# Performance work log

Measured on AMD Instinct MI355X. Metric: run time of the kernel, lower is better.

## Reference

```python
import jax, jax.numpy as jnp
import numpy as np

TEMPERATURE = 1.0
EPS = 1e-7
MAX_NORM = 0.9  # project points strictly inside the Poincare ball


def _project_ball(x):
    n = jnp.linalg.norm(x, axis=-1, keepdims=True)
    return x * jnp.minimum(1.0, MAX_NORM / jnp.maximum(n, EPS))


def setup_inputs() -> dict:
    key = jax.random.key(0)
    kq, kk, kv = jax.random.split(key, 3)
    B, Nq, Nk, D, V = 8, 2048, 2048, 64, 128
    queries = _project_ball(jax.random.normal(kq, (B, Nq, D), dtype=jnp.float32))
    keys = _project_ball(jax.random.normal(kk, (B, Nk, D), dtype=jnp.float32))
    values = jax.random.normal(kv, (B, Nk, V), dtype=jnp.float32)
    return {"queries": queries, "keys": keys, "values": values}


def _poincare_pairwise_dist(x, y):
    # x: (B,N,D), y: (B,M,D) -> (B,N,M) geodesic distances on the Poincare ball
    x2 = jnp.sum(x * x, axis=-1)            # (B,N)
    y2 = jnp.sum(y * y, axis=-1)            # (B,M)
    xy = jnp.einsum('bnd,bmd->bnm', x, y)   # (B,N,M)
    sq = jnp.maximum(x2[:, :, None] + y2[:, None, :] - 2.0 * xy, 0.0)
    denom = jnp.maximum((1.0 - x2)[:, :, None] * (1.0 - y2)[:, None, :], EPS)
    arg = 1.0 + 2.0 * sq / denom
    return jnp.arccosh(jnp.maximum(arg, 1.0 + EPS))


def reference(queries, keys, values):
    distances = _poincare_pairwise_dist(queries, keys)          # (B,Nq,Nk)
    scores = -(distances * distances) / TEMPERATURE
    attention_weights = jax.nn.softmax(scores, axis=-1)         # (B,Nq,Nk)
    output = jnp.einsum('bnm,bmv->bnv', attention_weights, values)  # (B,Nq,V)
    return output, attention_weights
```

## Files before the change

### kernel.cpp

```cpp
#include <hip/hip_runtime.h>
#include <math.h>

#define BB 8
#define NQ 2048
#define NK 2048
#define DD 64
#define VV 128
#define EPSF 1e-7f
#define NT3 (NK / 64)
#define FIXROWS 1024

typedef _Float16 half_t;
typedef half_t half8 __attribute__((ext_vector_type(8)));
typedef float  floatx4 __attribute__((ext_vector_type(4)));

__device__ __forceinline__ float score_exp(float x2, float y2, float xy)
{
    float sq = fmaf(-2.f, xy, x2 + y2);
    float dn = fmaxf((1.f - x2) * (1.f - y2), EPSF);
    float tt = fmaxf(2.f * sq * __builtin_amdgcn_rcpf(dn), EPSF);
    float u  = tt + __builtin_amdgcn_sqrtf(fmaf(tt, tt, tt + tt));
    float L  = __log2f(1.f + u);
    return __builtin_amdgcn_exp2f(-0.6931471805599453f * L * L);
}

__device__ __forceinline__ half8 cvt8(float4 a, float4 b)
{
    half8 h;
    h[0] = (half_t)a.x; h[1] = (half_t)a.y; h[2] = (half_t)a.z; h[3] = (half_t)a.w;
    h[4] = (half_t)b.x; h[5] = (half_t)b.y; h[6] = (half_t)b.z; h[7] = (half_t)b.w;
    return h;
}

__device__ __forceinline__ size_t khg_idx(int b, int tile, int f, int l)
{ return (((size_t)b * NT3 + tile) * 8 + f) * 64 + l; }
__device__ __forceinline__ size_t vhg_idx(int b, int tile, int f, int l)
{ return (((size_t)b * NT3 + tile) * 16 + f) * 64 + l; }

__device__ __forceinline__ int ssh_byte(int row, int col)
{
    return ((row << 7) + (col << 1)) ^ ((row & 7) << 4);
}

__global__ __launch_bounds__(256)
void k0_prep(const float* __restrict__ Q, const float* __restrict__ Kp,
             const float* __restrict__ V, half8* __restrict__ Khg,
             half8* __restrict__ Vhg, float* __restrict__ y2g,
             float* __restrict__ x2g, float* __restrict__ wsY,
             float* __restrict__ wsX)
{
    __shared__ float sVt[64 * VV];

    const int t = threadIdx.x, b = blockIdx.y, tile = blockIdx.x;
    const int kt = tile * 64;
    const float* Kb = Kp + (size_t)b * NK * DD;
    const float* Qb = Q  + (size_t)b * NQ * DD;
    const float* Vb = V  + (size_t)b * NK * VV;

#pragma unroll
    for (int i = 0; i < 8; ++i)
        ((float4*)sVt)[t + i * 256] = ((const float4*)(Vb + (size_t)kt * VV))[t + i * 256];

#pragma unroll
    for (int i = 0; i < 2; ++i) {
        int s = t + i * 256, f = s >> 6, l = s & 63;
        int krow = kt + (f >> 1) * 16 + (l & 15);
        int dcol = (f & 1) * 32 + (l >> 4) * 8;
        const float4* kp = (const float4*)(Kb + (size_t)krow * DD + dcol);
        Khg[khg_idx(b, tile, f, l)] = cvt8(kp[0], kp[1]);
    }
    if (t < 64) {
        const float4* kr = (const float4*)(Kb + (size_t)(kt + t) * DD);
        float s = 0.f;
#pragma unroll
        for (int i = 0; i < 16; ++i) {
            float4 v = kr[i];
            s = fmaf(v.x,v.x,s); s = fmaf(v.y,v.y,s);
            s = fmaf(v.z,v.z,s); s = fmaf(v.w,v.w,s);
        }
        y2g[(size_t)b * NK + kt + t] = s;
        if (b == 0) wsY[kt + t] = s;
    } else if (t < 128) {
        int r = t - 64;
        const float4* qr = (const float4*)(Qb + (size_t)(kt + r) * DD);
        float s = 0.f;
#pragma unroll
        for (int i = 0; i < 16; ++i) {
            float4 v = qr[i];
            s = fmaf(v.x,v.x,s); s = fmaf(v.y,v.y,s);
            s = fmaf(v.z,v.z,s); s = fmaf(v.w,v.w,s);
        }
        x2g[(size_t)b * NQ + kt + r] = s;
        if (b == 0) wsX[kt + r] = s;
    }
    __syncthreads();

#pragma unroll
    for (int i = 0; i < 4; ++i) {
        int s = t + i * 256, f = s >> 6, l = s & 63;
        int krow_l = (f & 1) * 32 + (l >> 4) * 8;
        int vcol   = (f >> 1) * 16 + (l & 15);
        half8 h;
#pragma unroll
        for (int j = 0; j < 8; ++j) h[j] = (half_t)sVt[(krow_l + j) * VV + vcol];
        Vhg[vhg_idx(b, tile, f, l)] = h;
    }
}

__global__ __launch_bounds__(512, 4)
void k_main(const float* __restrict__ Q, const half8* __restrict__ Khg,
            const half8* __restrict__ Vhg, const float* __restrict__ y2g,
            const float* __restrict__ x2g, float* __restrict__ W,
            float* __restrict__ O, float* __restrict__ RS)
{
    __shared__ half_t sSh[32 * 64];
    __shared__ float  y2k[NK];
    __shared__ float  part[4][32];
    __shared__ float  rsumS[32];

    const int t = threadIdx.x, w = t >> 6, lane = t & 63;
    const int n = lane & 15, quad = lane >> 4;
    const int qh = w & 1, kq = w >> 1;

    const int bid = blockIdx.x;
    const int swz = (bid & 7) * 64 + (bid >> 3);
    const int b = swz >> 6, qb = (swz & 63) * 32;
    const bool wskip = (b == 0) && (qb < FIXROWS);

    const float* Qb = Q + (size_t)b * NQ * DD;

    ((float4*)y2k)[t] = ((const float4*)(y2g + (size_t)b * NK))[t];

    half8 af[2];
#pragma unroll
    for (int ds = 0; ds < 2; ++ds) {
        const float4* qp = (const float4*)(Qb + (size_t)(qb + qh*16 + n) * DD + ds*32 + quad*8);
        af[ds] = cvt8(qp[0], qp[1]);
    }
    float x2r[4];
#pragma unroll
    for (int r = 0; r < 4; ++r)
        x2r[r] = x2g[(size_t)b * NQ + qb + qh * 16 + quad * 4 + r];
    __syncthreads();

    float srow[4] = {0.f, 0.f, 0.f, 0.f};

    half8 bf[8];
#pragma unroll
    for (int f = 0; f < 8; ++f) bf[f] = Khg[khg_idx(b, kq * 8, f, lane)];

#pragma unroll 1
    for (int kt0 = 0; kt0 < 512; kt0 += 64) {
        const bool pf = (kt0 + 64) < 512;
        half8 bfn[8];
        if (pf) {
#pragma unroll
            for (int f = 0; f < 8; ++f)
                bfn[f] = Khg[khg_idx(b, kq * 8 + ((kt0 + 64) >> 6), f, lane)];
        }

        floatx4 acc4[4] = {};
#pragma unroll
        for (int nt = 0; nt < 4; ++nt)
#pragma unroll
            for (int ds = 0; ds < 2; ++ds)
                acc4[nt] = __builtin_amdgcn_mfma_f32_16x16x32_f16(
                    af[ds], bf[nt * 2 + ds], acc4[nt], 0, 0, 0);

#pragma unroll
        for (int nt = 0; nt < 4; ++nt) {
            int lcol = kq * 512 + kt0 + nt * 16 + n;
            float y2 = y2k[lcol];
#pragma unroll
            for (int r = 0; r < 4; ++r)
                srow[r] += score_exp(x2r[r], y2, acc4[nt][r]);
        }
        if (pf) {
#pragma unroll
            for (int f = 0; f < 8; ++f) bf[f] = bfn[f];
        }
    }

#pragma unroll
    for (int off = 1; off < 16; off <<= 1)
#pragma unroll
        for (int r = 0; r < 4; ++r) srow[r] += __shfl_xor(srow[r], off);
    if (n == 0)
#pragma unroll
        for (int r = 0; r < 4; ++r) part[kq][qh * 16 + quad * 4 + r] = srow[r];
    __syncthreads();
    if (t < 32) {
        float s = (part[0][t] + part[1][t]) + (part[2][t] + part[3][t]);
        RS[(size_t)b * NQ + qb + t] = s;
        rsumS[t] = s;
    }
    __syncthreads();

    float rlr[4];
#pragma unroll
    for (int r = 0; r < 4; ++r)
        rlr[r] = __builtin_amdgcn_rcpf(rsumS[qh * 16 + quad * 4 + r]);

    float* Wb = W + (size_t)b * NQ * NK;
    floatx4 acc[2] = {};

    half8 kf[2];
#pragma unroll
    for (int ds = 0; ds < 2; ++ds) kf[ds] = Khg[khg_idx(b, 0, kq * 2 + ds, lane)];

#pragma unroll 1
    for (int tt = 0; tt < NT3; ++tt) {
        const bool pf = (tt + 1) < NT3;

        floatx4 a2 = {};
        a2 = __builtin_amdgcn_mfma_f32_16x16x32_f16(af[0], kf[0], a2, 0, 0, 0);
        a2 = __builtin_amdgcn_mfma_f32_16x16x32_f16(af[1], kf[1], a2, 0, 0, 0);

        half8 vf[4];
        vf[0] = Vhg[vhg_idx(b, tt, kq * 2,           lane)];
        vf[1] = Vhg[vhg_idx(b, tt, kq * 2 + 1,       lane)];
        vf[2] = Vhg[vhg_idx(b, tt, (kq + 4) * 2,     lane)];
        vf[3] = Vhg[vhg_idx(b, tt, (kq + 4) * 2 + 1, lane)];
        half8 kfn[2];
        if (pf) {
#pragma unroll
            for (int ds = 0; ds < 2; ++ds)
                kfn[ds] = Khg[khg_idx(b, tt + 1, kq * 2 + ds, lane)];
        }

        {
            int col  = kq * 16 + n;
            int gcol = tt * 64 + col;
            float y2 = y2k[gcol];
#pragma unroll
            for (int r = 0; r < 4; ++r) {
                float e  = score_exp(x2r[r], y2, a2[r]);
                float wv = e * rlr[r];
                int row = qh * 16 + quad * 4 + r;
                if (!wskip)
                    __builtin_nontemporal_store(wv, Wb + (size_t)(qb + row) * NK + gcol);
                *(half_t*)((char*)sSh + ssh_byte(row, col)) = (half_t)wv;
            }
        }
        __syncthreads();

        const int row2 = qh * 16 + n;
        half8 a0 = *(const half8*)((const char*)sSh + ssh_byte(row2, quad * 8));
        half8 a1 = *(const half8*)((const char*)sSh + ssh_byte(row2, 32 + quad * 8));
        acc[0] = __builtin_amdgcn_mfma_f32_16x16x32_f16(a0, vf[0], acc[0], 0, 0, 0);
        acc[0] = __builtin_amdgcn_mfma_f32_16x16x32_f16(a1, vf[1], acc[0], 0, 0, 0);
        acc[1] = __builtin_amdgcn_mfma_f32_16x16x32_f16(a0, vf[2], acc[1], 0, 0, 0);
        acc[1] = __builtin_amdgcn_mfma_f32_16x16x32_f16(a1, vf[3], acc[1], 0, 0, 0);
        __syncthreads();

        if (pf) { kf[0] = kfn[0]; kf[1] = kfn[1]; }
    }

    float* Ob = O + (size_t)b * NQ * VV;
#pragma unroll
    for (int ci = 0; ci < 2; ++ci) {
        int c = kq + ci * 4;
#pragma unroll
        for (int r = 0; r < 4; ++r)
            Ob[(size_t)(qb + qh * 16 + quad * 4 + r) * VV + c * 16 + n]
                = acc[ci][r];
    }
}

__global__ __launch_bounds__(256)
void k4_wfix(const float* __restrict__ Q, const float* __restrict__ Kp,
             const float* __restrict__ RS, const float* __restrict__ wsY,
             const float* __restrict__ wsX, float* __restrict__ W)
{
    __shared__ half8 sB[8 * 64];
    __shared__ float y2k[128];
    __shared__ float x2q[32];

    const int t = threadIdx.x, w = t >> 6, lane = t & 63;
    const int n = lane & 15, quad = lane >> 4;
    const int qh = w & 1, kn = w >> 1;
    const int qb = blockIdx.x * 32;
    const int kz = blockIdx.y * 128;

    if (t < 128) y2k[t] = wsY[kz + t];
    if (t < 32)  x2q[t] = wsX[qb + t];
    __syncthreads();

    half8 af[2];
#pragma unroll
    for (int ds = 0; ds < 2; ++ds) {
        const float4* qp = (const float4*)(Q + (size_t)(qb + qh*16 + n) * DD + ds*32 + quad*8);
        af[ds] = cvt8(qp[0], qp[1]);
    }
    float x2r[4], rlr[4];
#pragma unroll
    for (int r = 0; r < 4; ++r) {
        int row = qb + qh * 16 + quad * 4 + r;
        x2r[r] = x2q[qh * 16 + quad * 4 + r];
        rlr[r] = __builtin_amdgcn_rcpf(RS[row]);
    }

#pragma unroll 1
    for (int kt = 0; kt < 128; kt += 64) {
        __syncthreads();
#pragma unroll
        for (int i = 0; i < 2; ++i) {
            int s = t + i * 256, f = s >> 6, l = s & 63;
            int krow = kz + kt + (f >> 1) * 16 + (l & 15);
            int dcol = (f & 1) * 32 + (l >> 4) * 8;
            const float4* kp = (const float4*)(Kp + (size_t)krow * DD + dcol);
            sB[f * 64 + l] = cvt8(kp[0], kp[1]);
        }
        __syncthreads();

        floatx4 a2[2] = {};
#pragma unroll
        for (int nt = 0; nt < 2; ++nt)
#pragma unroll
            for (int ds = 0; ds < 2; ++ds)
                a2[nt] = __builtin_amdgcn_mfma_f32_16x16x32_f16(
                    af[ds], sB[((kn * 2 + nt) * 2 + ds) * 64 + lane], a2[nt], 0, 0, 0);

#pragma unroll
        for (int nt = 0; nt < 2; ++nt) {
            int col = kn * 32 + nt * 16 + n;
            float y2 = y2k[kt + col];
#pragma unroll
            for (int r = 0; r < 4; ++r) {
                float e = score_exp(x2r[r], y2, a2[nt][r]);
                int row = qh * 16 + quad * 4 + r;
                W[(size_t)(qb + row) * NK + kz + kt + col] = e * rlr[r];
            }
        }
    }
}

extern "C" void kernel_launch(void* const* d_in, const int* in_sizes, int n_in,
                              void* d_out, int out_size, void* d_ws, size_t ws_size,
                              hipStream_t stream)
{
    const float* Q  = (const float*)d_in[0];
    const float* Kp = (const float*)d_in[1];
    const float* Vp = (const float*)d_in[2];

    float* O     = (float*)d_out;
    float* attnW = O + (size_t)BB * NQ * VV;

    half8* Khg = (half8*)attnW;
    half8* Vhg = Khg + (size_t)BB * NT3 * 8 * 64;
    float* y2g = (float*)(Vhg + (size_t)BB * NT3 * 16 * 64);
    float* x2g = y2g + (size_t)BB * NK;

    float* RS  = (float*)d_ws;
    float* wsY = RS  + (size_t)BB * NQ;
    float* wsX = wsY + NK;

    k0_prep<<<dim3(NK / 64, BB),      256, 0, stream>>>(Q, Kp, Vp, Khg, Vhg, y2g, x2g, wsY, wsX);
    k_main <<<dim3(BB * (NQ / 32)),   512, 0, stream>>>(Q, Khg, Vhg, y2g, x2g, attnW, O, RS);
    k4_wfix<<<dim3(FIXROWS / 32, 16), 256, 0, stream>>>(Q, Kp, RS, wsY, wsX, attnW);
}
```

Measured before the change: 209.7 us.

## Store unnormalized exps in pass one and read them back for normalization

When the workspace is large enough, the staged K/V halves and norms go into the workspace instead of the output buffer, so the separate fix-up kernel is dropped. The first pass writes unnormalized exponentials to W, and the second pass reads them back, scales them, stores them and feeds them to the PV MFMA, which avoids recomputing QK and the score function. In exchange there is an extra full write and read of the 128MB attention matrix, which may cost more memory bandwidth than the recompute it saves. The old path is kept as a fallback when the workspace is too small.

```diff
diff --git a/kernel.cpp b/kernel.cpp
--- a/kernel.cpp
+++ b/kernel.cpp
@@ -11,6 +11,7 @@
 #define FIXROWS 1024
 
 typedef _Float16 half_t;
+typedef half_t half4 __attribute__((ext_vector_type(4)));
 typedef half_t half8 __attribute__((ext_vector_type(8)));
 typedef float  floatx4 __attribute__((ext_vector_type(4)));
 
@@ -107,11 +108,12 @@
     }
 }
 
+template<int READBACK>
 __global__ __launch_bounds__(512, 4)
-void k_main(const float* __restrict__ Q, const half8* __restrict__ Khg,
-            const half8* __restrict__ Vhg, const float* __restrict__ y2g,
-            const float* __restrict__ x2g, float* __restrict__ W,
-            float* __restrict__ O, float* __restrict__ RS)
+void k_main_t(const float* __restrict__ Q, const half8* __restrict__ Khg,
+              const half8* __restrict__ Vhg, const float* __restrict__ y2g,
+              const float* __restrict__ x2g, float* __restrict__ W,
+              float* __restrict__ O, float* __restrict__ RS, int fixrows)
 {
     __shared__ half_t sSh[32 * 64];
     __shared__ float  y2k[NK];
@@ -125,7 +127,7 @@
     const int bid = blockIdx.x;
     const int swz = (bid & 7) * 64 + (bid >> 3);
     const int b = swz >> 6, qb = (swz & 63) * 32;
-    const bool wskip = (b == 0) && (qb < FIXROWS);
+    const bool wskip = (!READBACK) && (b == 0) && (qb < fixrows);
 
     const float* Qb = Q + (size_t)b * NQ * DD;
 
@@ -143,6 +145,7 @@
         x2r[r] = x2g[(size_t)b * NQ + qb + qh * 16 + quad * 4 + r];
     __syncthreads();
 
+    float* WbE = W + (size_t)b * NQ * NK + (size_t)qb * NK;
     float srow[4] = {0.f, 0.f, 0.f, 0.f};
 
     half8 bf[8];
@@ -172,14 +175,19 @@
             int lcol = kq * 512 + kt0 + nt * 16 + n;
             float y2 = y2k[lcol];
 #pragma unroll
-            for (int r = 0; r < 4; ++r)
-                srow[r] += score_exp(x2r[r], y2, acc4[nt][r]);
+            for (int r = 0; r < 4; ++r) {
+                float e = score_exp(x2r[r], y2, acc4[nt][r]);
+                srow[r] += e;
+                if (READBACK)
+                    WbE[(size_t)(qh * 16 + quad * 4 + r) * NK + lcol] = e;
+            }
         }
         if (pf) {
 #pragma unroll
             for (int f = 0; f < 8; ++f) bf[f] = bfn[f];
         }
     }
+    if (READBACK) __threadfence();
 
 #pragma unroll
     for (int off = 1; off < 16; off <<= 1)
@@ -196,64 +204,99 @@
     }
     __syncthreads();
 
-    float rlr[4];
-#pragma unroll
-    for (int r = 0; r < 4; ++r)
-        rlr[r] = __builtin_amdgcn_rcpf(rsumS[qh * 16 + quad * 4 + r]);
-
+    floatx4 acc[2] = {};
     float* Wb = W + (size_t)b * NQ * NK;
-    floatx4 acc[2] = {};
-
-    half8 kf[2];
-#pragma unroll
-    for (int ds = 0; ds < 2; ++ds) kf[ds] = Khg[khg_idx(b, 0, kq * 2 + ds, lane)];
+
+    if (READBACK) {
+        const int erow = t >> 4, ec4 = (t & 15) * 4;
+        const float rl2 = __builtin_amdgcn_rcpf(rsumS[erow]);
+        float* Er = Wb + (size_t)(qb + erow) * NK;
 
 #pragma unroll 1
-    for (int tt = 0; tt < NT3; ++tt) {
-        const bool pf = (tt + 1) < NT3;
-
-        floatx4 a2 = {};
-        a2 = __builtin_amdgcn_mfma_f32_16x16x32_f16(af[0], kf[0], a2, 0, 0, 0);
-        a2 = __builtin_amdgcn_mfma_f32_16x16x32_f16(af[1], kf[1], a2, 0, 0, 0);
-
-        half8 vf[4];
-        vf[0] = Vhg[vhg_idx(b, tt, kq * 2,           lane)];
-        vf[1] = Vhg[vhg_idx(b, tt, kq * 2 + 1,       lane)];
-        vf[2] = Vhg[vhg_idx(b, tt, (kq + 4) * 2,     lane)];
-        vf[3] = Vhg[vhg_idx(b, tt, (kq + 4) * 2 + 1, lane)];
-        half8 kfn[2];
-        if (pf) {
-#pragma unroll
-            for (int ds = 0; ds < 2; ++ds)
-                kfn[ds] = Khg[khg_idx(b, tt + 1, kq * 2 + ds, lane)];
-        }
-
-        {
-            int col  = kq * 16 + n;
-            int gcol = tt * 64 + col;
-            float y2 = y2k[gcol];
-#pragma unroll
-            for (int r = 0; r < 4; ++r) {
-                float e  = score_exp(x2r[r], y2, a2[r]);
-                float wv = e * rlr[r];
-                int row = qh * 16 + quad * 4 + r;
-                if (!wskip)
-                    __builtin_nontemporal_store(wv, Wb + (size_t)(qb + row) * NK + gcol);
-                *(half_t*)((char*)sSh + ssh_byte(row, col)) = (half_t)wv;
+        for (int tt = 0; tt < NT3; ++tt) {
+            half8 vf[4];
+            vf[0] = Vhg[vhg_idx(b, tt, kq * 2,           lane)];
+            vf[1] = Vhg[vhg_idx(b, tt, kq * 2 + 1,       lane)];
+            vf[2] = Vhg[vhg_idx(b, tt, (kq + 4) * 2,     lane)];
+            vf[3] = Vhg[vhg_idx(b, tt, (kq + 4) * 2 + 1, lane)];
+
+            floatx4 e4 = *(const floatx4*)(Er + tt * 64 + ec4);
+            floatx4 wv4;
+            wv4[0] = e4[0] * rl2; wv4[1] = e4[1] * rl2;
+            wv4[2] = e4[2] * rl2; wv4[3] = e4[3] * rl2;
+            __builtin_nontemporal_store(wv4, (floatx4*)(Er + tt * 64 + ec4));
+            half4 h;
+            h[0] = (half_t)wv4[0]; h[1] = (half_t)wv4[1];
+            h[2] = (half_t)wv4[2]; h[3] = (half_t)wv4[3];
+            *(half4*)((char*)sSh + ssh_byte(erow, ec4)) = h;
+            __syncthreads();
+
+            const int row2 = qh * 16 + n;
+            half8 a0 = *(const half8*)((const char*)sSh + ssh_byte(row2, quad * 8));
+            half8 a1 = *(const half8*)((const char*)sSh + ssh_byte(row2, 32 + quad * 8));
+            acc[0] = __builtin_amdgcn_mfma_f32_16x16x32_f16(a0, vf[0], acc[0], 0, 0, 0);
+            acc[0] = __builtin_amdgcn_mfma_f32_16x16x32_f16(a1, vf[1], acc[0], 0, 0, 0);
+            acc[1] = __builtin_amdgcn_mfma_f32_16x16x32_f16(a0, vf[2], acc[1], 0, 0, 0);
+            acc[1] = __builtin_amdgcn_mfma_f32_16x16x32_f16(a1, vf[3], acc[1], 0, 0, 0);
+            __syncthreads();
+        }
+    } else {
+        float rlr[4];
+#pragma unroll
+        for (int r = 0; r < 4; ++r)
+            rlr[r] = __builtin_amdgcn_rcpf(rsumS[qh * 16 + quad * 4 + r]);
+
+        half8 kf[2];
+#pragma unroll
+        for (int ds = 0; ds < 2; ++ds) kf[ds] = Khg[khg_idx(b, 0, kq * 2 + ds, lane)];
+
+#pragma unroll 1
+        for (int tt = 0; tt < NT3; ++tt) {
+            const bool pf = (tt + 1) < NT3;
+
+            floatx4 a2 = {};
+            a2 = __builtin_amdgcn_mfma_f32_16x16x32_f16(af[0], kf[0], a2, 0, 0, 0);
+            a2 = __builtin_amdgcn_mfma_f32_16x16x32_f16(af[1], kf[1], a2, 0, 0, 0);
+
+            half8 vf[4];
+            vf[0] = Vhg[vhg_idx(b, tt, kq * 2,           lane)];
+            vf[1] = Vhg[vhg_idx(b, tt, kq * 2 + 1,       lane)];
+            vf[2] = Vhg[vhg_idx(b, tt, (kq + 4) * 2,     lane)];
+            vf[3] = Vhg[vhg_idx(b, tt, (kq + 4) * 2 + 1, lane)];
+            half8 kfn[2];
+            if (pf) {
+#pragma unroll
+                for (int ds = 0; ds < 2; ++ds)
+                    kfn[ds] = Khg[khg_idx(b, tt + 1, kq * 2 + ds, lane)];
             }
-        }
-        __syncthreads();
-
-        const int row2 = qh * 16 + n;
-        half8 a0 = *(const half8*)((const char*)sSh + ssh_byte(row2, quad * 8));
-        half8 a1 = *(const half8*)((const char*)sSh + ssh_byte(row2, 32 + quad * 8));
-        acc[0] = __builtin_amdgcn_mfma_f32_16x16x32_f16(a0, vf[0], acc[0], 0, 0, 0);
-        acc[0] = __builtin_amdgcn_mfma_f32_16x16x32_f16(a1, vf[1], acc[0], 0, 0, 0);
-        acc[1] = __builtin_amdgcn_mfma_f32_16x16x32_f16(a0, vf[2], acc[1], 0, 0, 0);
-        acc[1] = __builtin_amdgcn_mfma_f32_16x16x32_f16(a1, vf[3], acc[1], 0, 0, 0);
-        __syncthreads();
-
-        if (pf) { kf[0] = kfn[0]; kf[1] = kfn[1]; }
+
+            {
+                int col  = kq * 16 + n;
+                int gcol = tt * 64 + col;
+                float y2 = y2k[gcol];
+#pragma unroll
+                for (int r = 0; r < 4; ++r) {
+                    float e  = score_exp(x2r[r], y2, a2[r]);
+                    float wv = e * rlr[r];
+                    int row = qh * 16 + quad * 4 + r;
+                    if (!wskip)
+                        __builtin_nontemporal_store(wv, Wb + (size_t)(qb + row) * NK + gcol);
+                    *(half_t*)((char*)sSh + ssh_byte(row, col)) = (half_t)wv;
+                }
+            }
+            __syncthreads();
+
+            const int row2 = qh * 16 + n;
+            half8 a0 = *(const half8*)((const char*)sSh + ssh_byte(row2, quad * 8));
+            half8 a1 = *(const half8*)((const char*)sSh + ssh_byte(row2, 32 + quad * 8));
+            acc[0] = __builtin_amdgcn_mfma_f32_16x16x32_f16(a0, vf[0], acc[0], 0, 0, 0);
+            acc[0] = __builtin_amdgcn_mfma_f32_16x16x32_f16(a1, vf[1], acc[0], 0, 0, 0);
+            acc[1] = __builtin_amdgcn_mfma_f32_16x16x32_f16(a0, vf[2], acc[1], 0, 0, 0);
+            acc[1] = __builtin_amdgcn_mfma_f32_16x16x32_f16(a1, vf[3], acc[1], 0, 0, 0);
+            __syncthreads();
+
+            if (pf) { kf[0] = kfn[0]; kf[1] = kfn[1]; }
+        }
     }
 
     float* Ob = O + (size_t)b * NQ * VV;
@@ -346,16 +389,36 @@
     float* O     = (float*)d_out;
     float* attnW = O + (size_t)BB * NQ * VV;
 
-    half8* Khg = (half8*)attnW;
-    half8* Vhg = Khg + (size_t)BB * NT3 * 8 * 64;
-    float* y2g = (float*)(Vhg + (size_t)BB * NT3 * 16 * 64);
-    float* x2g = y2g + (size_t)BB * NK;
-
-    float* RS  = (float*)d_ws;
-    float* wsY = RS  + (size_t)BB * NQ;
-    float* wsX = wsY + NK;
-
-    k0_prep<<<dim3(NK / 64, BB),      256, 0, stream>>>(Q, Kp, Vp, Khg, Vhg, y2g, x2g, wsY, wsX);
-    k_main <<<dim3(BB * (NQ / 32)),   512, 0, stream>>>(Q, Khg, Vhg, y2g, x2g, attnW, O, RS);
-    k4_wfix<<<dim3(FIXROWS / 32, 16), 256, 0, stream>>>(Q, Kp, RS, wsY, wsX, attnW);
-}
+    const size_t nKH = (size_t)BB * NT3 * 8  * 64;
+    const size_t nVH = (size_t)BB * NT3 * 16 * 64;
+    const size_t need = nKH * sizeof(half8) + nVH * sizeof(half8)
+                      + (size_t)(BB * NK + 2 * BB * NQ) * sizeof(float);
+
+    if (ws_size >= need) {
+        half8* Khg = (half8*)d_ws;
+        half8* Vhg = Khg + nKH;
+        float* y2g = (float*)(Vhg + nVH);
+        float* x2g = y2g + (size_t)BB * NK;
+        float* RS  = x2g + (size_t)BB * NQ;
+
+        k0_prep<<<dim3(NK / 64, BB), 256, 0, stream>>>(Q, Kp, Vp, Khg, Vhg,
+                                                       y2g, x2g, y2g, x2g);
+        k_main_t<1><<<dim3(BB * (NQ / 32)), 512, 0, stream>>>(
+            Q, Khg, Vhg, y2g, x2g, attnW, O, RS, 0);
+    } else {
+        half8* Khg = (half8*)attnW;
+        half8* Vhg = Khg + nKH;
+        float* y2g = (float*)(Vhg + nVH);
+        float* x2g = y2g + (size_t)BB * NK;
+
+        float* RS  = (float*)d_ws;
+        float* wsY = RS  + (size_t)BB * NQ;
+        float* wsX = wsY + NK;
+
+        k0_prep<<<dim3(NK / 64, BB), 256, 0, stream>>>(Q, Kp, Vp, Khg, Vhg,
+                                                       y2g, x2g, wsY, wsX);
+        k_main_t<0><<<dim3(BB * (NQ / 32)), 512, 0, stream>>>(
+            Q, Khg, Vhg, y2g, x2g, attnW, O, RS, FIXROWS);
+        k4_wfix<<<dim3(FIXROWS / 32, 16), 256, 0, stream>>>(Q, Kp, RS, wsY, wsX, attnW);
+    }
+}
```

New measurement: 344.7 us. +64.4%, slower.
